# Optimization experiments

Hardware: AMD Instinct MI355X
Metric: run time of the kernel (lower is better)

## Reference

```python
import jax, jax.numpy as jnp
import numpy as np

BS = 4
D = 256
N3 = BS * 80 * 80   # 25600 level-3 nodes
N4 = BS * 40 * 40   # 6400  level-4 nodes
N5 = BS * 20 * 20   # 1600  level-5 nodes
N = N3 + N4 + N5    # 33600 total graph nodes
EC = 260000         # contextual-graph edges (~8-neighborhood lattice)
EH = 120000         # hierarchical-graph edges (cross-scale)


def setup_inputs() -> dict:
    key = jax.random.key(0)
    ks = jax.random.split(key, 16)
    f = lambda k, s: jax.random.normal(k, s, dtype=jnp.float32) * 0.05
    return {
        # backbone features (yolov8-l channel widths)
        'c3': f(ks[0], (BS, 256, 80, 80)),
        'c4': f(ks[1], (BS, 512, 40, 40)),
        'c5': f(ks[2], (BS, 512, 20, 20)),
        # lateral 1x1 convs (stored as [out, in] since kernel is 1x1)
        'w3_1x1': f(ks[3], (256, 256)), 'b3_1x1': jnp.zeros((256,), jnp.float32),
        'w4_1x1': f(ks[4], (256, 512)), 'b4_1x1': jnp.zeros((256,), jnp.float32),
        'w5_1x1': f(ks[5], (256, 512)), 'b5_1x1': jnp.zeros((256,), jnp.float32),
        # output 3x3 convs
        'w3_3x3': f(ks[6], (256, 256, 3, 3)), 'b3_3x3': jnp.zeros((256,), jnp.float32),
        'w4_3x3': f(ks[7], (256, 256, 3, 3)), 'b4_3x3': jnp.zeros((256,), jnp.float32),
        'w5_3x3': f(ks[8], (256, 256, 3, 3)), 'b5_3x3': jnp.zeros((256,), jnp.float32),
        # 6 contextual + 3 hierarchical GNN layers (stacked)
        'Wc': f(ks[9], (6, 256, 256)), 'bc': jnp.zeros((6, 256), jnp.float32),
        'Wh': f(ks[10], (3, 256, 256)), 'bh': jnp.zeros((3, 256), jnp.float32),
        # edge lists (src -> dst message direction)
        'src_c': jax.random.randint(ks[11], (EC,), 0, N, dtype=jnp.int32),
        'dst_c': jax.random.randint(ks[12], (EC,), 0, N, dtype=jnp.int32),
        'src_h': jax.random.randint(ks[13], (EH,), 0, N, dtype=jnp.int32),
        'dst_h': jax.random.randint(ks[14], (EH,), 0, N, dtype=jnp.int32),
    }


def _conv1x1(x, w, b):
    return jnp.einsum('bchw,oc->bohw', x, w) + b[None, :, None, None]


def _conv3x3(x, w, b):
    y = jax.lax.conv_general_dilated(x, w, (1, 1), 'SAME')
    return y + b[None, :, None, None]


def _up2(x):
    return jnp.repeat(jnp.repeat(x, 2, axis=2), 2, axis=3)


def _degree(dst):
    d = jax.ops.segment_sum(jnp.ones(dst.shape, jnp.float32), dst, num_segments=N)
    return jnp.maximum(d, 1.0)[:, None]


def _gnn_layer(h, W, b, src, dst, deg):
    # gather-aggregate-scatter: mean over incoming messages + self, then linear+relu
    agg = jax.ops.segment_sum(h[src], dst, num_segments=N) / deg  # [N, D]
    return jax.nn.relu((h + agg) @ W + b)


def reference(c3, c4, c5,
              w3_1x1, b3_1x1, w4_1x1, b4_1x1, w5_1x1, b5_1x1,
              w3_3x3, b3_3x3, w4_3x3, b4_3x3, w5_3x3, b5_3x3,
              Wc, bc, Wh, bh,
              src_c, dst_c, src_h, dst_h):
    p3 = _conv1x1(c3, w3_1x1, b3_1x1)  # [BS,256,80,80]
    p4 = _conv1x1(c4, w4_1x1, b4_1x1)  # [BS,256,40,40]
    p5 = _conv1x1(c5, w5_1x1, b5_1x1)  # [BS,256,20,20]

    # CNN -> graph node features (NHWC flatten, cat levels)
    h = jnp.concatenate([
        p3.transpose(0, 2, 3, 1).reshape(-1, D),
        p4.transpose(0, 2, 3, 1).reshape(-1, D),
        p5.transpose(0, 2, 3, 1).reshape(-1, D),
    ], axis=0)  # [N, 256]

    deg_c = _degree(dst_c)
    deg_h = _degree(dst_h)
    for i in range(3):                       # context1..3
        h = _gnn_layer(h, Wc[i], bc[i], src_c, dst_c, deg_c)
    for i in range(3):                       # hierarch1..3
        h = _gnn_layer(h, Wh[i], bh[i], src_h, dst_h, deg_h)
    for i in range(3, 6):                    # context4..6
        h = _gnn_layer(h, Wc[i], bc[i], src_c, dst_c, deg_c)

    # graph -> CNN
    p3g = h[:N3].reshape(BS, 80, 80, D).transpose(0, 3, 1, 2)
    p4g = h[N3:N3 + N4].reshape(BS, 40, 40, D).transpose(0, 3, 1, 2)
    p5g = h[N3 + N4:].reshape(BS, 20, 20, D).transpose(0, 3, 1, 2)

    p5 = p5 + p5g
    p4 = p4 + _up2(p5) + p4g
    p3 = p3 + _up2(p4) + p3g

    out3 = _conv3x3(p3, w3_3x3, b3_3x3)
    out4 = _conv3x3(p4, w4_3x3, b4_3x3)
    out5 = _conv3x3(p5, w5_3x3, b5_3x3)
    return out3, out4, out5
```

## Files before the change

kernel.cpp:

```cpp
#include <hip/hip_runtime.h>
#include <stdint.h>

#define N3i 25600
#define N4i 6400
#define N5i 1600
#define NNi 33600
#define ECi 260000
#define EHi 120000

typedef unsigned short u16;
typedef __bf16 bf16x8 __attribute__((ext_vector_type(8)));
typedef float f32x4 __attribute__((ext_vector_type(4)));
typedef unsigned short u16x8 __attribute__((ext_vector_type(8)));

__device__ __forceinline__ float b2f(u16 u) {
    union { float f; uint32_t i; } v; v.i = ((uint32_t)u) << 16; return v.f;
}
__device__ __forceinline__ u16 f2b(float f) {
    union { float f; uint32_t i; } v; v.f = f;
    uint32_t x = v.i;
    uint32_t r = (x + 0x7FFFu + ((x >> 16) & 1u)) >> 16;
    return (u16)r;
}

__device__ __forceinline__ void gll16(const u16* g, u16* l) {
    __builtin_amdgcn_global_load_lds((const __attribute__((address_space(1))) void*)g,
                                     (__attribute__((address_space(3))) void*)l, 16, 0, 0);
}

__global__ void detect_kernel(const void* __restrict__ c3raw, int* __restrict__ flag,
                              uint32_t* __restrict__ zp) {
    const uint32_t* p = (const uint32_t*)c3raw;
    int t = threadIdx.x;
    zp[t] = 0;
    int vote = 0;
    for (int i = t; i < 256; i += 64) {
        uint32_t w = p[i];
        uint32_t lo = w & 0xFFFFu;
        uint32_t e = (lo >> 7) & 0xFFu;
        if (lo == 0u || (e >= 100u && e <= 127u)) vote++;
    }
#pragma unroll
    for (int d = 32; d >= 1; d >>= 1) vote += __shfl_down(vote, d, 64);
    if (t == 0) flag[0] = (vote >= 192) ? 1 : 0;
}

__global__ void zero_i32(int* p, int n) {
    int i = blockIdx.x * 256 + threadIdx.x;
    if (i < n) p[i] = 0;
}

__global__ void hist2_kernel(const int* __restrict__ dst_c, const int* __restrict__ dst_h,
                             int* __restrict__ cnt_c, int* __restrict__ cnt_h) {
    int i = blockIdx.x * 256 + threadIdx.x;
    if (i < ECi) {
        int d = dst_c[i];
        if ((unsigned)d < (unsigned)NNi) atomicAdd(&cnt_c[d], 1);
    } else {
        int j = i - ECi;
        if (j < EHi) {
            int d = dst_h[j];
            if ((unsigned)d < (unsigned)NNi) atomicAdd(&cnt_h[d], 1);
        }
    }
}

__global__ __launch_bounds__(1024) void scan2_kernel(
    const int* __restrict__ cnt_c, int* __restrict__ rs_c, int* __restrict__ cur_c,
    float* __restrict__ inv_c,
    const int* __restrict__ cnt_h, int* __restrict__ rs_h, int* __restrict__ cur_h,
    float* __restrict__ inv_h, int n) {
    const int* cnt = blockIdx.x ? cnt_h : cnt_c;
    int* rs = blockIdx.x ? rs_h : rs_c;
    int* cur = blockIdx.x ? cur_h : cur_c;
    float* inv = blockIdx.x ? inv_h : inv_c;
    __shared__ int ws[16];
    __shared__ int base;
    int t = threadIdx.x, wid = t >> 6, lane = t & 63;
    if (t == 0) { base = 0; rs[0] = 0; }
    __syncthreads();
    for (int i0 = 0; i0 < n; i0 += 1024) {
        int i = i0 + t;
        int v = (i < n) ? cnt[i] : 0;
        int x = v;
#pragma unroll
        for (int d = 1; d < 64; d <<= 1) {
            int y = __shfl_up(x, d, 64);
            if (lane >= d) x += y;
        }
        if (lane == 63) ws[wid] = x;
        __syncthreads();
        if (wid == 0) {
            int s = (lane < 16) ? ws[lane] : 0;
#pragma unroll
            for (int d = 1; d < 16; d <<= 1) {
                int y = __shfl_up(s, d, 64);
                if (lane >= d) s += y;
            }
            if (lane < 16) ws[lane] = s;
        }
        __syncthreads();
        int b = base;
        int incl = x + (wid ? ws[wid - 1] : 0);
        if (i < n) {
            rs[i + 1] = b + incl;
            cur[i] = b + incl - v;
            int dv = v < 1 ? 1 : v;
            inv[i] = 1.0f / (float)dv;
        }
        int tot = ws[15];
        __syncthreads();
        if (t == 1023) base = b + tot;
        __syncthreads();
    }
}

__global__ void fill2_kernel(const int* __restrict__ src_c, const int* __restrict__ dst_c,
                             int* __restrict__ cur_c, int* __restrict__ csr_c,
                             const int* __restrict__ src_h, const int* __restrict__ dst_h,
                             int* __restrict__ cur_h, int* __restrict__ csr_h) {
    int i = blockIdx.x * 256 + threadIdx.x;
    if (i < ECi) {
        int d = dst_c[i];
        if ((unsigned)d < (unsigned)NNi) {
            int p = atomicAdd(&cur_c[d], 1);
            if ((unsigned)p < (unsigned)ECi) csr_c[p] = src_c[i];
        }
    } else {
        int j = i - ECi;
        if (j < EHi) {
            int d = dst_h[j];
            if ((unsigned)d < (unsigned)NNi) {
                int p = atomicAdd(&cur_h[d], 1);
                if ((unsigned)p < (unsigned)EHi) csr_h[p] = src_h[j];
            }
        }
    }
}

struct CvtJobs { const void* src[11]; u16* dst[11]; int n[11]; };

__global__ void cvt_all_kernel(CvtJobs j, const int* __restrict__ flag) {
    int job = blockIdx.y;
    int i = blockIdx.x * 256 + threadIdx.x;
    if (i >= j.n[job]) return;
    const void* s = j.src[job];
    j.dst[job][i] = flag[0] ? ((const u16*)s)[i] : f2b(((const float*)s)[i]);
}

__device__ __forceinline__ void tin_body(const void* in, size_t ioff, u16* outp, int R, int C,
                                         int isb, int c0, int r0, u16 (*tile)[33]) {
    const u16* inb = (const u16*)in + ioff;
    const float* inf_ = (const float*)in + ioff;
    int tx = threadIdx.x, ty = threadIdx.y;
#pragma unroll
    for (int i = 0; i < 4; i++) {
        int r = r0 + ty + i * 8, c = c0 + tx;
        if (r < R && c < C) {
            size_t idx = (size_t)r * C + c;
            tile[ty + i * 8][tx] = isb ? inb[idx] : f2b(inf_[idx]);
        }
    }
    __syncthreads();
#pragma unroll
    for (int i = 0; i < 4; i++) {
        int c = c0 + ty + i * 8, r = r0 + tx;
        if (c < C && r < R) outp[(size_t)c * R + r] = tile[tx][ty + i * 8];
    }
}

__global__ void transpose_in3(const void* __restrict__ c3, const void* __restrict__ c4,
                              const void* __restrict__ c5, u16* __restrict__ Xt3,
                              u16* __restrict__ Xt4, u16* __restrict__ Xt5,
                              const int* __restrict__ flag) {
    __shared__ u16 tile[32][33];
    int bx = blockIdx.x;
    const void* in; u16* outb; int R, C, xb;
    if (bx < 200)      { in = c3; outb = Xt3; R = 256; C = 6400; xb = bx; }
    else if (bx < 250) { in = c4; outb = Xt4; R = 512; C = 1600; xb = bx - 200; }
    else               { in = c5; outb = Xt5; R = 512; C = 400;  xb = bx - 250; }
    int r0 = blockIdx.y * 32;
    if (r0 >= R) return;
    size_t boff = (size_t)blockIdx.z * R * C;
    tin_body(in, boff, outb + boff, R, C, flag[0], xb * 32, r0, tile);
}

__global__ void transpose_w(const void* __restrict__ Wc, const void* __restrict__ Wh,
                            u16* __restrict__ WtG, const int* __restrict__ flag) {
    __shared__ u16 tile[32][33];
    int z = blockIdx.z;
    const void* in = (z < 6) ? Wc : Wh;
    int zi = (z < 6) ? z : z - 6;
    tin_body(in, (size_t)zi * 65536, WtG + (size_t)z * 65536, 256, 256, flag[0],
             blockIdx.x * 32, blockIdx.y * 32, tile);
}

__global__ void transpose_out3(const u16* __restrict__ OutT, void* __restrict__ outv,
                               const int* __restrict__ flag) {
    __shared__ u16 tile[32][33];
    int by = blockIdx.y;
    const u16* inb; size_t out_off; int R, yb;
    if (by < 200)      { inb = OutT; out_off = 0; R = 6400; yb = by; }
    else if (by < 250) { inb = OutT + (size_t)N3i * 256; out_off = (size_t)4 * 256 * 6400; R = 1600; yb = by - 200; }
    else               { inb = OutT + (size_t)(N3i + N4i) * 256; out_off = (size_t)4 * 256 * 8000; R = 400; yb = by - 250; }
    int r0 = yb * 32;
    if (r0 >= R) return;
    const int C = 256;
    int isb = flag[0];
    int c0 = blockIdx.x * 32;
    size_t boff = (size_t)blockIdx.z * R * C;
    const u16* inp = inb + boff;
    int tx = threadIdx.x, ty = threadIdx.y;
#pragma unroll
    for (int i = 0; i < 4; i++) {
        int r = r0 + ty + i * 8, c = c0 + tx;
        if (r < R && c < C) tile[ty + i * 8][tx] = inp[(size_t)r * C + c];
    }
    __syncthreads();
#pragma unroll
    for (int i = 0; i < 4; i++) {
        int c = c0 + ty + i * 8, r = r0 + tx;
        if (c < C && r < R) {
            size_t o = out_off + boff + (size_t)c * R + r;
            u16 v = tile[tx][ty + i * 8];
            if (isb) ((u16*)outv)[o] = v;
            else ((float*)outv)[o] = b2f(v);
        }
    }
}

__global__ void convw3_kernel(const void* __restrict__ w0, const void* __restrict__ w1,
                              const void* __restrict__ w2, u16* __restrict__ WtC,
                              const int* __restrict__ flag) {
    int lvl = blockIdx.y;
    const void* w = (lvl == 0) ? w0 : (lvl == 1) ? w1 : w2;
    u16* wt = WtC + (size_t)lvl * 256 * 2304;
    int i = blockIdx.x * 256 + threadIdx.x;
    if (i >= 256 * 2304) return;
    int n = i / 2304;
    int k = i - n * 2304;
    int tap = k >> 8, ci = k & 255;
    int si = n * 2304 + ci * 9 + tap;
    wt[i] = flag[0] ? ((const u16*)w)[si] : f2b(((const float*)w)[si]);
}

__global__ __launch_bounds__(256) void gather_kernel(
    const u16* __restrict__ H, const int* __restrict__ csr, const int* __restrict__ rs,
    const float* __restrict__ invdeg, u16* __restrict__ T, int ecap) {
    int node = blockIdx.x * 4 + (threadIdx.x >> 6);
    if (node >= NNi) return;
    int lane = threadIdx.x & 63;
    int half = lane >> 5;
    int c = (lane & 31) * 8;
    int e0 = rs[node], e1 = rs[node + 1];
    e0 = e0 < 0 ? 0 : e0;
    e1 = e1 > ecap ? ecap : e1;
    const u16* Hn = H + (size_t)node * 256 + c;
    u16x8 self = *(const u16x8*)Hn;
    float a0 = 0.f, a1 = 0.f, a2 = 0.f, a3 = 0.f, a4 = 0.f, a5 = 0.f, a6 = 0.f, a7 = 0.f;
    float b0 = 0.f, b1 = 0.f, b2 = 0.f, b3 = 0.f, b4 = 0.f, b5 = 0.f, b6 = 0.f, b7 = 0.f;
    int e = e0 + half;
    while (e + 2 < e1) {
        int i0 = csr[e];
        int i1 = csr[e + 2];
        i0 = ((unsigned)i0 < (unsigned)NNi) ? i0 : 0;
        i1 = ((unsigned)i1 < (unsigned)NNi) ? i1 : 0;
        u16x8 h0 = *(const u16x8*)(H + (size_t)i0 * 256 + c);
        u16x8 h1 = *(const u16x8*)(H + (size_t)i1 * 256 + c);
        a0 += b2f(h0[0]); a1 += b2f(h0[1]); a2 += b2f(h0[2]); a3 += b2f(h0[3]);
        a4 += b2f(h0[4]); a5 += b2f(h0[5]); a6 += b2f(h0[6]); a7 += b2f(h0[7]);
        b0 += b2f(h1[0]); b1 += b2f(h1[1]); b2 += b2f(h1[2]); b3 += b2f(h1[3]);
        b4 += b2f(h1[4]); b5 += b2f(h1[5]); b6 += b2f(h1[6]); b7 += b2f(h1[7]);
        e += 4;
    }
    if (e < e1) {
        int i0 = csr[e];
        i0 = ((unsigned)i0 < (unsigned)NNi) ? i0 : 0;
        u16x8 h0 = *(const u16x8*)(H + (size_t)i0 * 256 + c);
        a0 += b2f(h0[0]); a1 += b2f(h0[1]); a2 += b2f(h0[2]); a3 += b2f(h0[3]);
        a4 += b2f(h0[4]); a5 += b2f(h0[5]); a6 += b2f(h0[6]); a7 += b2f(h0[7]);
    }
    a0 += b0; a1 += b1; a2 += b2; a3 += b3; a4 += b4; a5 += b5; a6 += b6; a7 += b7;
    a0 += __shfl_xor(a0, 32, 64); a1 += __shfl_xor(a1, 32, 64);
    a2 += __shfl_xor(a2, 32, 64); a3 += __shfl_xor(a3, 32, 64);
    a4 += __shfl_xor(a4, 32, 64); a5 += __shfl_xor(a5, 32, 64);
    a6 += __shfl_xor(a6, 32, 64); a7 += __shfl_xor(a7, 32, 64);
    if (half == 0) {
        float inv = invdeg[node];
        u16x8 o;
        o[0] = f2b(b2f(self[0]) + a0 * inv); o[1] = f2b(b2f(self[1]) + a1 * inv);
        o[2] = f2b(b2f(self[2]) + a2 * inv); o[3] = f2b(b2f(self[3]) + a3 * inv);
        o[4] = f2b(b2f(self[4]) + a4 * inv); o[5] = f2b(b2f(self[5]) + a5 * inv);
        o[6] = f2b(b2f(self[6]) + a6 * inv); o[7] = f2b(b2f(self[7]) + a7 * inv);
        *(u16x8*)(T + (size_t)node * 256 + c) = o;
    }
}

template <bool CONV, bool RELU>
__device__ __forceinline__ void gemm_body(
    u16 (* __restrict__ lds)[4096],
    const u16* __restrict__ A, int lda,
    const u16* __restrict__ Bt, int ldb,
    const u16* __restrict__ bias,
    const u16* __restrict__ zp,
    u16* __restrict__ out, u16* __restrict__ out2,
    int M, int K, int H, int W, int m0, int n0) {
    int t = threadIdx.x;
    int w = t >> 6, lane = t & 63;
    int wm = w & 1, wn = w >> 1;
    f32x4 acc[4][4] = {};

    int g0 = w * 128 + lane;
    int g1 = g0 + 64;
    int row0 = g0 >> 2, c0 = g0 & 3;
    int row1 = g1 >> 2, c1 = g1 & 3;
    int ss0 = ((c0 ^ ((row0 >> 1) & 3)) << 3);
    int ss1 = ((c1 ^ ((row1 >> 1) & 3)) << 3);

    int ar0 = m0 + row0, ar1 = m0 + row1;
    bool aok0 = ar0 < M, aok1 = ar1 < M;
    int y0_ = 0, x0_ = 0, y1_ = 0, x1_ = 0;
    if (CONV) {
        int HW = H * W;
        if (aok0) { int b = ar0 / HW; int rem = ar0 - b * HW; y0_ = rem / W; x0_ = rem - y0_ * W; }
        if (aok1) { int b = ar1 / HW; int rem = ar1 - b * HW; y1_ = rem / W; x1_ = rem - y1_ * W; }
    }
    const u16* aP0 = A + (size_t)ar0 * lda + ss0;
    const u16* aP1 = A + (size_t)ar1 * lda + ss1;
    const u16* bP0 = Bt + (size_t)(n0 + row0) * ldb + ss0;
    const u16* bP1 = Bt + (size_t)(n0 + row1) * ldb + ss1;

    int lbase = w * 1024;

    auto stage = [&](int bf, int ks) {
        int k0 = ks << 5;
        u16* LA = lds[bf * 2];
        u16* LB = lds[bf * 2 + 1];
        const u16* sa0;
        const u16* sa1;
        if (!CONV) {
            sa0 = aok0 ? aP0 + k0 : zp;
            sa1 = aok1 ? aP1 + k0 : zp;
        } else {
            int tap = k0 >> 8;
            int t3 = tap / 3;
            int dy = t3 - 1, dx = tap - t3 * 3 - 1;
            int off = (dy * W + dx) * lda + (k0 & 255);
            int yy0 = y0_ + dy, xx0 = x0_ + dx;
            int yy1 = y1_ + dy, xx1 = x1_ + dx;
            sa0 = (aok0 && (unsigned)yy0 < (unsigned)H && (unsigned)xx0 < (unsigned)W) ? aP0 + off : zp;
            sa1 = (aok1 && (unsigned)yy1 < (unsigned)H && (unsigned)xx1 < (unsigned)W) ? aP1 + off : zp;
        }
        gll16(sa0, LA + lbase);
        gll16(sa1, LA + lbase + 512);
        gll16(bP0 + k0, LB + lbase);
        gll16(bP1 + k0, LB + lbase + 512);
    };

    int nst = K >> 5;
    int fm = lane & 15;
    int co = (((lane >> 4) ^ ((fm >> 1) & 3)) << 3);

    stage(0, 0);
    stage(1, 1);
    for (int s = 0; s < nst; s++) {
        int bf = s % 3;
        if (s + 1 < nst) {
            asm volatile("s_waitcnt vmcnt(4)" ::: "memory");
        } else {
            asm volatile("s_waitcnt vmcnt(0)" ::: "memory");
        }
        __builtin_amdgcn_s_barrier();
        if (s + 2 < nst) stage((s + 2) % 3, s + 2);
        const u16* LA = lds[bf * 2];
        const u16* LB = lds[bf * 2 + 1];
        bf16x8 af[4], bfv[4];
#pragma unroll
        for (int i = 0; i < 4; i++) af[i] = *(const bf16x8*)&LA[(wm * 64 + i * 16 + fm) * 32 + co];
#pragma unroll
        for (int j = 0; j < 4; j++) bfv[j] = *(const bf16x8*)&LB[(wn * 64 + j * 16 + fm) * 32 + co];
        __builtin_amdgcn_s_setprio(1);
#pragma unroll
        for (int i = 0; i < 4; i++)
#pragma unroll
            for (int j = 0; j < 4; j++)
                acc[i][j] = __builtin_amdgcn_mfma_f32_16x16x32_bf16(af[i], bfv[j], acc[i][j], 0, 0, 0);
        __builtin_amdgcn_s_setprio(0);
    }

    int q = lane >> 4, nl = lane & 15;
#pragma unroll
    for (int j = 0; j < 4; j++) {
        int n = n0 + wn * 64 + j * 16 + nl;
        float bv = b2f(bias[n]);
#pragma unroll
        for (int i = 0; i < 4; i++) {
            int mbase = m0 + wm * 64 + i * 16 + q * 4;
#pragma unroll
            for (int rg = 0; rg < 4; rg++) {
                int m = mbase + rg;
                if (m < M) {
                    float v = acc[i][j][rg] + bv;
                    if (RELU) v = fmaxf(v, 0.f);
                    u16 bs = f2b(v);
                    out[(size_t)m * 256 + n] = bs;
                    if (out2) out2[(size_t)m * 256 + n] = bs;
                }
            }
        }
    }
}

template <bool CONV, bool RELU>
__global__ __launch_bounds__(256) void gemm_kernel(
    const u16* __restrict__ A, int lda,
    const u16* __restrict__ Bt, int ldb,
    const u16* __restrict__ bias,
    const u16* __restrict__ zp,
    u16* __restrict__ out, u16* __restrict__ out2,
    int M, int K, int H, int W) {
    __shared__ __align__(16) u16 lds[6][4096];
    gemm_body<CONV, RELU>(lds, A, lda, Bt, ldb, bias, zp, out, out2, M, K, H, W,
                          blockIdx.y * 128, blockIdx.x * 128);
}

__global__ __launch_bounds__(256) void lat_all_kernel(
    const u16* __restrict__ Xt3, const u16* __restrict__ Xt4, const u16* __restrict__ Xt5,
    const u16* __restrict__ W1, const u16* __restrict__ BB, const u16* __restrict__ zp,
    u16* __restrict__ P, u16* __restrict__ Ha) {
    __shared__ __align__(16) u16 lds[6][4096];
    int by = blockIdx.y;
    const u16* A; const u16* Bt; const u16* bias;
    int K, Ml, m0; size_t off;
    if (by < 200)      { A = Xt3; Bt = W1;          bias = BB;       K = 256; Ml = N3i; off = 0;                          m0 = by * 128; }
    else if (by < 250) { A = Xt4; Bt = W1 + 65536;  bias = BB + 256; K = 512; Ml = N4i; off = (size_t)N3i * 256;          m0 = (by - 200) * 128; }
    else               { A = Xt5; Bt = W1 + 196608; bias = BB + 512; K = 512; Ml = N5i; off = (size_t)(N3i + N4i) * 256;  m0 = (by - 250) * 128; }
    gemm_body<false, false>(lds, A, K, Bt, K, bias, zp, P + off, Ha + off, Ml, K, 0, 0,
                            m0, blockIdx.x * 128);
}

__global__ __launch_bounds__(256) void conv_gemm_all(
    const u16* __restrict__ Pc, const u16* __restrict__ WtC,
    const u16* __restrict__ BB, const u16* __restrict__ zp, u16* __restrict__ OutT) {
    __shared__ __align__(16) u16 lds[6][4096];
    int by = blockIdx.y;
    int lvl, yl, Hd, Ml; size_t base;
    if (by < 200)      { lvl = 0; yl = by;       Hd = 80; Ml = N3i; base = 0; }
    else if (by < 250) { lvl = 1; yl = by - 200; Hd = 40; Ml = N4i; base = (size_t)N3i * 256; }
    else               { lvl = 2; yl = by - 250; Hd = 20; Ml = N5i; base = (size_t)(N3i + N4i) * 256; }
    gemm_body<true, false>(lds, Pc + base, 256, WtC + (size_t)lvl * 256 * 2304, 2304,
                           BB + 3072 + lvl * 256, zp, OutT + base, nullptr,
                           Ml, 2304, Hd, Hd, yl * 128, blockIdx.x * 128);
}

__global__ void pyr_kernel(const u16* __restrict__ P, const u16* __restrict__ Hf,
                           u16* __restrict__ Pc) {
    int i = blockIdx.x * 256 + threadIdx.x;
    if (i >= NNi * 64) return;
    int node = i >> 6, c = (i & 63) * 4;
    size_t bi = (size_t)node * 256 + c;
    ushort4 pv = *(const ushort4*)(P + bi);
    ushort4 hv = *(const ushort4*)(Hf + bi);
    float v0 = b2f(pv.x) + b2f(hv.x);
    float v1 = b2f(pv.y) + b2f(hv.y);
    float v2 = b2f(pv.z) + b2f(hv.z);
    float v3 = b2f(pv.w) + b2f(hv.w);
    if (node < N3i) {
        int b = node / 6400, rem = node - b * 6400;
        int y = rem / 80, x = rem - y * 80;
        size_t s4 = ((size_t)N3i + b * 1600 + (y >> 1) * 40 + (x >> 1)) * 256 + c;
        size_t s5 = ((size_t)(N3i + N4i) + b * 400 + (y >> 2) * 20 + (x >> 2)) * 256 + c;
        ushort4 p4 = *(const ushort4*)(P + s4), h4 = *(const ushort4*)(Hf + s4);
        ushort4 p5 = *(const ushort4*)(P + s5), h5 = *(const ushort4*)(Hf + s5);
        v0 += b2f(p4.x) + b2f(h4.x) + b2f(p5.x) + b2f(h5.x);
        v1 += b2f(p4.y) + b2f(h4.y) + b2f(p5.y) + b2f(h5.y);
        v2 += b2f(p4.z) + b2f(h4.z) + b2f(p5.z) + b2f(h5.z);
        v3 += b2f(p4.w) + b2f(h4.w) + b2f(p5.w) + b2f(h5.w);
    } else if (node < N3i + N4i) {
        int n4 = node - N3i;
        int b = n4 / 1600, rem = n4 - b * 1600;
        int y = rem / 40, x = rem - y * 40;
        size_t s5 = ((size_t)(N3i + N4i) + b * 400 + (y >> 1) * 20 + (x >> 1)) * 256 + c;
        ushort4 p5 = *(const ushort4*)(P + s5), h5 = *(const ushort4*)(Hf + s5);
        v0 += b2f(p5.x) + b2f(h5.x);
        v1 += b2f(p5.y) + b2f(h5.y);
        v2 += b2f(p5.z) + b2f(h5.z);
        v3 += b2f(p5.w) + b2f(h5.w);
    }
    ushort4 o;
    o.x = f2b(v0); o.y = f2b(v1); o.z = f2b(v2); o.w = f2b(v3);
    *(ushort4*)(Pc + bi) = o;
}

extern "C" void kernel_launch(void* const* d_in, const int* in_sizes, int n_in,
                              void* d_out, int out_size, void* d_ws, size_t ws_size,
                              hipStream_t stream) {
    (void)in_sizes; (void)n_in; (void)out_size; (void)ws_size;
    const void* c3 = d_in[0];
    const void* c4 = d_in[1];
    const void* c5 = d_in[2];
    const void* w3_1 = d_in[3];
    const void* b3_1 = d_in[4];
    const void* w4_1 = d_in[5];
    const void* b4_1 = d_in[6];
    const void* w5_1 = d_in[7];
    const void* b5_1 = d_in[8];
    const void* w3_3 = d_in[9];
    const void* b3_3 = d_in[10];
    const void* w4_3 = d_in[11];
    const void* b4_3 = d_in[12];
    const void* w5_3 = d_in[13];
    const void* b5_3 = d_in[14];
    const void* Wc = d_in[15];
    const void* bc = d_in[16];
    const void* Wh = d_in[17];
    const void* bh = d_in[18];
    const int* src_c = (const int*)d_in[19];
    const int* dst_c = (const int*)d_in[20];
    const int* src_h = (const int*)d_in[21];
    const int* dst_h = (const int*)d_in[22];

    char* w = (char*)d_ws;
    auto alloc = [&](size_t bytes) -> void* {
        void* p = (void*)w;
        w += (bytes + 255) & ~(size_t)255;
        return p;
    };
    u16* XT  = (u16*)alloc(((size_t)N3i * 256 + (size_t)N4i * 512 + (size_t)N5i * 512) * 2);
    u16* Xt3 = XT;
    u16* Xt4 = XT + (size_t)N3i * 256;
    u16* Xt5 = Xt4 + (size_t)N4i * 512;
    u16* T   = XT;
    u16* Pc  = XT;
    u16* WtC = XT + (size_t)NNi * 256;
    u16* WtG = (u16*)alloc((size_t)9 * 65536 * 2);
    u16* W1  = (u16*)alloc((size_t)(65536 + 131072 + 131072) * 2);
    u16* BB  = (u16*)alloc((size_t)3840 * 2);
    u16* P   = (u16*)alloc((size_t)NNi * 256 * 2);
    u16* Ha  = (u16*)alloc((size_t)NNi * 256 * 2);
    u16* Hb  = (u16*)d_out;
    int* csr_c = (int*)alloc((size_t)ECi * 4);
    int* csr_h = (int*)alloc((size_t)EHi * 4);
    int* cnt2  = (int*)alloc((size_t)2 * NNi * 4);
    int* cnt_c = cnt2;
    int* cnt_h = cnt2 + NNi;
    int* rs_c  = (int*)alloc((size_t)(NNi + 1) * 4);
    int* rs_h  = (int*)alloc((size_t)(NNi + 1) * 4);
    int* cur_c = (int*)alloc((size_t)NNi * 4);
    int* cur_h = (int*)alloc((size_t)NNi * 4);
    float* inv_c = (float*)alloc((size_t)NNi * 4);
    float* inv_h = (float*)alloc((size_t)NNi * 4);
    int* flag  = (int*)alloc(256);
    u16* zp    = (u16*)alloc(256);

    detect_kernel<<<1, 64, 0, stream>>>(c3, flag, (uint32_t*)zp);

    zero_i32<<<(2 * NNi + 255) / 256, 256, 0, stream>>>(cnt2, 2 * NNi);
    hist2_kernel<<<(ECi + EHi + 255) / 256, 256, 0, stream>>>(dst_c, dst_h, cnt_c, cnt_h);
    scan2_kernel<<<2, 1024, 0, stream>>>(cnt_c, rs_c, cur_c, inv_c,
                                         cnt_h, rs_h, cur_h, inv_h, NNi);
    fill2_kernel<<<(ECi + EHi + 255) / 256, 256, 0, stream>>>(
        src_c, dst_c, cur_c, csr_c, src_h, dst_h, cur_h, csr_h);

    CvtJobs cj;
    cj.src[0] = w3_1; cj.dst[0] = W1;          cj.n[0] = 65536;
    cj.src[1] = w4_1; cj.dst[1] = W1 + 65536;  cj.n[1] = 131072;
    cj.src[2] = w5_1; cj.dst[2] = W1 + 196608; cj.n[2] = 131072;
    cj.src[3] = b3_1; cj.dst[3] = BB;          cj.n[3] = 256;
    cj.src[4] = b4_1; cj.dst[4] = BB + 256;    cj.n[4] = 256;
    cj.src[5] = b5_1; cj.dst[5] = BB + 512;    cj.n[5] = 256;
    cj.src[6] = bc;   cj.dst[6] = BB + 768;    cj.n[6] = 1536;
    cj.src[7] = bh;   cj.dst[7] = BB + 2304;   cj.n[7] = 768;
    cj.src[8] = b3_3; cj.dst[8] = BB + 3072;   cj.n[8] = 256;
    cj.src[9] = b4_3; cj.dst[9] = BB + 3328;   cj.n[9] = 256;
    cj.src[10] = b5_3; cj.dst[10] = BB + 3584; cj.n[10] = 256;
    cvt_all_kernel<<<dim3(512, 11), 256, 0, stream>>>(cj, flag);

    transpose_in3<<<dim3(263, 16, 4), dim3(32, 8), 0, stream>>>(c3, c4, c5, Xt3, Xt4, Xt5, flag);
    transpose_w<<<dim3(8, 8, 9), dim3(32, 8), 0, stream>>>(Wc, Wh, WtG, flag);

    lat_all_kernel<<<dim3(2, 263), 256, 0, stream>>>(Xt3, Xt4, Xt5, W1, BB, zp, P, Ha);

    convw3_kernel<<<dim3(2304, 3), 256, 0, stream>>>(w3_3, w4_3, w5_3, WtC, flag);

    u16* Hcur = Ha;
    u16* Hnxt = Hb;
    for (int l = 0; l < 9; l++) {
        bool ctx = (l < 3) || (l >= 6);
        const int* csr = ctx ? csr_c : csr_h;
        const int* rs = ctx ? rs_c : rs_h;
        const float* inv = ctx ? inv_c : inv_h;
        int ecap = ctx ? ECi : EHi;
        int wi = (l < 3) ? l : (l < 6 ? 6 + (l - 3) : l - 3);
        const u16* bias = (l < 3) ? BB + 768 + l * 256
                        : (l < 6 ? BB + 2304 + (l - 3) * 256 : BB + 768 + (l - 3) * 256);
        gather_kernel<<<(NNi + 3) / 4, 256, 0, stream>>>(Hcur, csr, rs, inv, T, ecap);
        gemm_kernel<false, true><<<dim3(2, 263), 256, 0, stream>>>(
            T, 256, WtG + (size_t)wi * 65536, 256, bias, zp, Hnxt, nullptr, NNi, 256, 0, 0);
        u16* tmp = Hcur; Hcur = Hnxt; Hnxt = tmp;
    }
    u16* OutT = Hnxt;

    pyr_kernel<<<(NNi * 64 + 255) / 256, 256, 0, stream>>>(P, Hcur, Pc);

    conv_gemm_all<<<dim3(2, 263), 256, 0, stream>>>(Pc, WtC, BB, zp, OutT);

    transpose_out3<<<dim3(8, 263, 4), dim3(32, 8), 0, stream>>>(OutT, d_out, flag);
}
```

Before: 698.3 us.

## Fuse GNN neighbor gather into GEMM via LDS-resident aggregated tile

Replaces the separate gather kernel and GEMM per GNN layer with one kernel: each block aggregates 64 nodes' neighbor features into a swizzled LDS tile, then multiplies by the full 256-wide weight with double-buffered weight staging and fused bias+ReLU. This removes the global round trip of the intermediate T buffer and one launch per layer. The gather loop is also unrolled to four loads in flight. Separately, the shared gemm_body pipeline is changed from triple-buffered with explicit vmcnt waits and setprio to double-buffered with __syncthreads, cutting LDS use but possibly exposing more load latency in the lateral and 3x3 conv GEMMs.

```diff
diff --git a/kernel.cpp b/kernel.cpp
--- a/kernel.cpp
+++ b/kernel.cpp
@@ -244,55 +244,129 @@
     wt[i] = flag[0] ? ((const u16*)w)[si] : f2b(((const float*)w)[si]);
 }
 
-__global__ __launch_bounds__(256) void gather_kernel(
+#define TSLAB 2064
+__global__ __launch_bounds__(256) void gnn_fused_kernel(
     const u16* __restrict__ H, const int* __restrict__ csr, const int* __restrict__ rs,
-    const float* __restrict__ invdeg, u16* __restrict__ T, int ecap) {
-    int node = blockIdx.x * 4 + (threadIdx.x >> 6);
-    if (node >= NNi) return;
-    int lane = threadIdx.x & 63;
+    const float* __restrict__ invdeg, const u16* __restrict__ Bt,
+    const u16* __restrict__ bias, u16* __restrict__ out, int ecap) {
+    __shared__ __align__(16) u16 Tl[8 * TSLAB];
+    __shared__ __align__(16) u16 LB[2][8192];
+    int t = threadIdx.x;
+    int w = t >> 6, lane = t & 63;
+    int m0 = blockIdx.x * 64;
+
+    int l2 = lane >> 2;
+    int q = lane & 3;
+    int srb = (l2 >> 1) & 3;
+    auto stageB = [&](int bf, int ks) {
+        int k0 = ks << 5;
+#pragma unroll
+        for (int j = 0; j < 4; j++) {
+            int row = w * 64 + j * 16 + l2;
+            const u16* src = Bt + (size_t)row * 256 + k0 + ((q ^ srb) << 3);
+            gll16(src, &LB[bf][(w * 64 + j * 16) * 32]);
+        }
+    };
+    stageB(0, 0);
+
     int half = lane >> 5;
-    int c = (lane & 31) * 8;
-    int e0 = rs[node], e1 = rs[node + 1];
-    e0 = e0 < 0 ? 0 : e0;
-    e1 = e1 > ecap ? ecap : e1;
-    const u16* Hn = H + (size_t)node * 256 + c;
-    u16x8 self = *(const u16x8*)Hn;
-    float a0 = 0.f, a1 = 0.f, a2 = 0.f, a3 = 0.f, a4 = 0.f, a5 = 0.f, a6 = 0.f, a7 = 0.f;
-    float b0 = 0.f, b1 = 0.f, b2 = 0.f, b3 = 0.f, b4 = 0.f, b5 = 0.f, b6 = 0.f, b7 = 0.f;
-    int e = e0 + half;
-    while (e + 2 < e1) {
-        int i0 = csr[e];
-        int i1 = csr[e + 2];
-        i0 = ((unsigned)i0 < (unsigned)NNi) ? i0 : 0;
-        i1 = ((unsigned)i1 < (unsigned)NNi) ? i1 : 0;
-        u16x8 h0 = *(const u16x8*)(H + (size_t)i0 * 256 + c);
-        u16x8 h1 = *(const u16x8*)(H + (size_t)i1 * 256 + c);
-        a0 += b2f(h0[0]); a1 += b2f(h0[1]); a2 += b2f(h0[2]); a3 += b2f(h0[3]);
-        a4 += b2f(h0[4]); a5 += b2f(h0[5]); a6 += b2f(h0[6]); a7 += b2f(h0[7]);
-        b0 += b2f(h1[0]); b1 += b2f(h1[1]); b2 += b2f(h1[2]); b3 += b2f(h1[3]);
-        b4 += b2f(h1[4]); b5 += b2f(h1[5]); b6 += b2f(h1[6]); b7 += b2f(h1[7]);
-        e += 4;
-    }
-    if (e < e1) {
-        int i0 = csr[e];
-        i0 = ((unsigned)i0 < (unsigned)NNi) ? i0 : 0;
-        u16x8 h0 = *(const u16x8*)(H + (size_t)i0 * 256 + c);
-        a0 += b2f(h0[0]); a1 += b2f(h0[1]); a2 += b2f(h0[2]); a3 += b2f(h0[3]);
-        a4 += b2f(h0[4]); a5 += b2f(h0[5]); a6 += b2f(h0[6]); a7 += b2f(h0[7]);
-    }
-    a0 += b0; a1 += b1; a2 += b2; a3 += b3; a4 += b4; a5 += b5; a6 += b6; a7 += b7;
-    a0 += __shfl_xor(a0, 32, 64); a1 += __shfl_xor(a1, 32, 64);
-    a2 += __shfl_xor(a2, 32, 64); a3 += __shfl_xor(a3, 32, 64);
-    a4 += __shfl_xor(a4, 32, 64); a5 += __shfl_xor(a5, 32, 64);
-    a6 += __shfl_xor(a6, 32, 64); a7 += __shfl_xor(a7, 32, 64);
-    if (half == 0) {
-        float inv = invdeg[node];
-        u16x8 o;
-        o[0] = f2b(b2f(self[0]) + a0 * inv); o[1] = f2b(b2f(self[1]) + a1 * inv);
-        o[2] = f2b(b2f(self[2]) + a2 * inv); o[3] = f2b(b2f(self[3]) + a3 * inv);
-        o[4] = f2b(b2f(self[4]) + a4 * inv); o[5] = f2b(b2f(self[5]) + a5 * inv);
-        o[6] = f2b(b2f(self[6]) + a6 * inv); o[7] = f2b(b2f(self[7]) + a7 * inv);
-        *(u16x8*)(T + (size_t)node * 256 + c) = o;
+    int ch = (lane & 31) * 8;
+    for (int ni = 0; ni < 16; ni++) {
+        int node = m0 + w * 16 + ni;
+        int e0 = rs[node], e1 = rs[node + 1];
+        e0 = e0 < 0 ? 0 : e0;
+        e1 = e1 > ecap ? ecap : e1;
+        u16x8 self = *(const u16x8*)(H + (size_t)node * 256 + ch);
+        float a0 = 0.f, a1 = 0.f, a2 = 0.f, a3 = 0.f, a4 = 0.f, a5 = 0.f, a6 = 0.f, a7 = 0.f;
+        float c0 = 0.f, c1 = 0.f, c2 = 0.f, c3 = 0.f, c4 = 0.f, c5 = 0.f, c6 = 0.f, c7 = 0.f;
+        int e = e0 + half;
+        while (e + 6 < e1) {
+            int i0 = csr[e], i1 = csr[e + 2], i2 = csr[e + 4], i3 = csr[e + 6];
+            i0 = ((unsigned)i0 < (unsigned)NNi) ? i0 : 0;
+            i1 = ((unsigned)i1 < (unsigned)NNi) ? i1 : 0;
+            i2 = ((unsigned)i2 < (unsigned)NNi) ? i2 : 0;
+            i3 = ((unsigned)i3 < (unsigned)NNi) ? i3 : 0;
+            u16x8 h0 = *(const u16x8*)(H + (size_t)i0 * 256 + ch);
+            u16x8 h1 = *(const u16x8*)(H + (size_t)i1 * 256 + ch);
+            u16x8 h2 = *(const u16x8*)(H + (size_t)i2 * 256 + ch);
+            u16x8 h3 = *(const u16x8*)(H + (size_t)i3 * 256 + ch);
+            a0 += b2f(h0[0]); a1 += b2f(h0[1]); a2 += b2f(h0[2]); a3 += b2f(h0[3]);
+            a4 += b2f(h0[4]); a5 += b2f(h0[5]); a6 += b2f(h0[6]); a7 += b2f(h0[7]);
+            c0 += b2f(h1[0]); c1 += b2f(h1[1]); c2 += b2f(h1[2]); c3 += b2f(h1[3]);
+            c4 += b2f(h1[4]); c5 += b2f(h1[5]); c6 += b2f(h1[6]); c7 += b2f(h1[7]);
+            a0 += b2f(h2[0]); a1 += b2f(h2[1]); a2 += b2f(h2[2]); a3 += b2f(h2[3]);
+            a4 += b2f(h2[4]); a5 += b2f(h2[5]); a6 += b2f(h2[6]); a7 += b2f(h2[7]);
+            c0 += b2f(h3[0]); c1 += b2f(h3[1]); c2 += b2f(h3[2]); c3 += b2f(h3[3]);
+            c4 += b2f(h3[4]); c5 += b2f(h3[5]); c6 += b2f(h3[6]); c7 += b2f(h3[7]);
+            e += 8;
+        }
+        while (e < e1) {
+            int i0 = csr[e];
+            i0 = ((unsigned)i0 < (unsigned)NNi) ? i0 : 0;
+            u16x8 h0 = *(const u16x8*)(H + (size_t)i0 * 256 + ch);
+            a0 += b2f(h0[0]); a1 += b2f(h0[1]); a2 += b2f(h0[2]); a3 += b2f(h0[3]);
+            a4 += b2f(h0[4]); a5 += b2f(h0[5]); a6 += b2f(h0[6]); a7 += b2f(h0[7]);
+            e += 2;
+        }
+        a0 += c0; a1 += c1; a2 += c2; a3 += c3; a4 += c4; a5 += c5; a6 += c6; a7 += c7;
+        a0 += __shfl_xor(a0, 32, 64); a1 += __shfl_xor(a1, 32, 64);
+        a2 += __shfl_xor(a2, 32, 64); a3 += __shfl_xor(a3, 32, 64);
+        a4 += __shfl_xor(a4, 32, 64); a5 += __shfl_xor(a5, 32, 64);
+        a6 += __shfl_xor(a6, 32, 64); a7 += __shfl_xor(a7, 32, 64);
+        if (half == 0) {
+            float inv = invdeg[node];
+            u16x8 o;
+            o[0] = f2b(b2f(self[0]) + a0 * inv); o[1] = f2b(b2f(self[1]) + a1 * inv);
+            o[2] = f2b(b2f(self[2]) + a2 * inv); o[3] = f2b(b2f(self[3]) + a3 * inv);
+            o[4] = f2b(b2f(self[4]) + a4 * inv); o[5] = f2b(b2f(self[5]) + a5 * inv);
+            o[6] = f2b(b2f(self[6]) + a6 * inv); o[7] = f2b(b2f(self[7]) + a7 * inv);
+            int r = w * 16 + ni;
+            int slab = (lane & 31) >> 2;
+            int qq = lane & 3;
+            int sr = (r >> 1) & 3;
+            *(u16x8*)(&Tl[slab * TSLAB + r * 32 + ((qq ^ sr) << 3)]) = o;
+        }
+    }
+    __syncthreads();
+
+    f32x4 acc[4][4] = {};
+    int fm = lane & 15;
+    int kq = lane >> 4;
+    int co = ((kq ^ ((fm >> 1) & 3)) << 3);
+    for (int s = 0; s < 8; s++) {
+        int bf = s & 1;
+        if (s + 1 < 8) stageB(bf ^ 1, s + 1);
+        bf16x8 af[4], bfv[4];
+#pragma unroll
+        for (int i = 0; i < 4; i++)
+            af[i] = *(const bf16x8*)&Tl[s * TSLAB + (i * 16 + fm) * 32 + co];
+#pragma unroll
+        for (int j = 0; j < 4; j++)
+            bfv[j] = *(const bf16x8*)&LB[bf][(w * 64 + j * 16 + fm) * 32 + co];
+#pragma unroll
+        for (int i = 0; i < 4; i++)
+#pragma unroll
+            for (int j = 0; j < 4; j++)
+                acc[i][j] = __builtin_amdgcn_mfma_f32_16x16x32_bf16(af[i], bfv[j], acc[i][j], 0, 0, 0);
+        __syncthreads();
+    }
+
+    int qd = lane >> 4, nl = lane & 15;
+#pragma unroll
+    for (int j = 0; j < 4; j++) {
+        int n = w * 64 + j * 16 + nl;
+        float bv = b2f(bias[n]);
+#pragma unroll
+        for (int i = 0; i < 4; i++) {
+            int mbase = i * 16 + qd * 4;
+#pragma unroll
+            for (int rg = 0; rg < 4; rg++) {
+                int m = mbase + rg;
+                float v = acc[i][j][rg] + bv;
+                v = fmaxf(v, 0.f);
+                out[(size_t)(m0 + m) * 256 + n] = f2b(v);
+            }
+        }
     }
 }
 
@@ -332,8 +406,7 @@
 
     int lbase = w * 1024;
 
-    auto stage = [&](int bf, int ks) {
-        int k0 = ks << 5;
+    auto stage = [&](int bf, int k0) {
         u16* LA = lds[bf * 2];
         u16* LB = lds[bf * 2 + 1];
         const u16* sa0;
@@ -362,16 +435,10 @@
     int co = (((lane >> 4) ^ ((fm >> 1) & 3)) << 3);
 
     stage(0, 0);
-    stage(1, 1);
+    __syncthreads();
     for (int s = 0; s < nst; s++) {
-        int bf = s % 3;
-        if (s + 1 < nst) {
-            asm volatile("s_waitcnt vmcnt(4)" ::: "memory");
-        } else {
-            asm volatile("s_waitcnt vmcnt(0)" ::: "memory");
-        }
-        __builtin_amdgcn_s_barrier();
-        if (s + 2 < nst) stage((s + 2) % 3, s + 2);
+        int bf = s & 1;
+        if (s + 1 < nst) stage(bf ^ 1, (s + 1) << 5);
         const u16* LA = lds[bf * 2];
         const u16* LB = lds[bf * 2 + 1];
         bf16x8 af[4], bfv[4];
@@ -379,13 +446,12 @@
         for (int i = 0; i < 4; i++) af[i] = *(const bf16x8*)&LA[(wm * 64 + i * 16 + fm) * 32 + co];
 #pragma unroll
         for (int j = 0; j < 4; j++) bfv[j] = *(const bf16x8*)&LB[(wn * 64 + j * 16 + fm) * 32 + co];
-        __builtin_amdgcn_s_setprio(1);
 #pragma unroll
         for (int i = 0; i < 4; i++)
 #pragma unroll
             for (int j = 0; j < 4; j++)
                 acc[i][j] = __builtin_amdgcn_mfma_f32_16x16x32_bf16(af[i], bfv[j], acc[i][j], 0, 0, 0);
-        __builtin_amdgcn_s_setprio(0);
+        __syncthreads();
     }
 
     int q = lane >> 4, nl = lane & 15;
@@ -411,24 +477,11 @@
     }
 }
 
-template <bool CONV, bool RELU>
-__global__ __launch_bounds__(256) void gemm_kernel(
-    const u16* __restrict__ A, int lda,
-    const u16* __restrict__ Bt, int ldb,
-    const u16* __restrict__ bias,
-    const u16* __restrict__ zp,
-    u16* __restrict__ out, u16* __restrict__ out2,
-    int M, int K, int H, int W) {
-    __shared__ __align__(16) u16 lds[6][4096];
-    gemm_body<CONV, RELU>(lds, A, lda, Bt, ldb, bias, zp, out, out2, M, K, H, W,
-                          blockIdx.y * 128, blockIdx.x * 128);
-}
-
 __global__ __launch_bounds__(256) void lat_all_kernel(
     const u16* __restrict__ Xt3, const u16* __restrict__ Xt4, const u16* __restrict__ Xt5,
     const u16* __restrict__ W1, const u16* __restrict__ BB, const u16* __restrict__ zp,
     u16* __restrict__ P, u16* __restrict__ Ha) {
-    __shared__ __align__(16) u16 lds[6][4096];
+    __shared__ __align__(16) u16 lds[4][4096];
     int by = blockIdx.y;
     const u16* A; const u16* Bt; const u16* bias;
     int K, Ml, m0; size_t off;
@@ -442,7 +495,7 @@
 __global__ __launch_bounds__(256) void conv_gemm_all(
     const u16* __restrict__ Pc, const u16* __restrict__ WtC,
     const u16* __restrict__ BB, const u16* __restrict__ zp, u16* __restrict__ OutT) {
-    __shared__ __align__(16) u16 lds[6][4096];
+    __shared__ __align__(16) u16 lds[4][4096];
     int by = blockIdx.y;
     int lvl, yl, Hd, Ml; size_t base;
     if (by < 200)      { lvl = 0; yl = by;       Hd = 80; Ml = N3i; base = 0; }
@@ -530,7 +583,6 @@
     u16* Xt3 = XT;
     u16* Xt4 = XT + (size_t)N3i * 256;
     u16* Xt5 = Xt4 + (size_t)N4i * 512;
-    u16* T   = XT;
     u16* Pc  = XT;
     u16* WtC = XT + (size_t)NNi * 256;
     u16* WtG = (u16*)alloc((size_t)9 * 65536 * 2);
@@ -594,9 +646,8 @@
         int wi = (l < 3) ? l : (l < 6 ? 6 + (l - 3) : l - 3);
         const u16* bias = (l < 3) ? BB + 768 + l * 256
                         : (l < 6 ? BB + 2304 + (l - 3) * 256 : BB + 768 + (l - 3) * 256);
-        gather_kernel<<<(NNi + 3) / 4, 256, 0, stream>>>(Hcur, csr, rs, inv, T, ecap);
-        gemm_kernel<false, true><<<dim3(2, 263), 256, 0, stream>>>(
-            T, 256, WtG + (size_t)wi * 65536, 256, bias, zp, Hnxt, nullptr, NNi, 256, 0, 0);
+        gnn_fused_kernel<<<NNi / 64, 256, 0, stream>>>(
+            Hcur, csr, rs, inv, WtG + (size_t)wi * 65536, bias, Hnxt, ecap);
         u16* tmp = Hcur; Hcur = Hnxt; Hnxt = tmp;
     }
     u16* OutT = Hnxt;
```

New measurement: 1.058 ms. 1.52x slower.
